# Optimization experiments

Measured on AMD Instinct MI355X. Metric: run time of the kernel, lower is better.

## Reference

```python
import jax, jax.numpy as jnp
import numpy as np

N = 100000   # nodes
E = 1600000  # edges (avg degree 16)
B = 64       # graphs in batch
D_IN = 64
D = 64       # d_model


def setup_inputs() -> dict:
    key = jax.random.key(0)
    ks = jax.random.split(key, 12)
    inp = {}
    inp["x_raw"] = jax.random.normal(ks[0], (N, D_IN), dtype=jnp.float32)
    inp["edge_index"] = jax.random.randint(ks[1], (2, E), 0, N)
    inp["batch"] = jnp.sort(jax.random.randint(ks[2], (N,), 0, B))
    # SAGEConv params per layer: lin_l (weight+bias, applied to neighbor mean),
    # lin_r (weight only, applied to root) -- PyG defaults.
    dins = [D_IN, D, D]
    for i, din in enumerate(dins):
        scale = 1.0 / np.sqrt(din)
        inp[f"Wl{i}"] = jax.random.normal(ks[3 + 3 * i], (D, din), dtype=jnp.float32) * scale
        inp[f"bl{i}"] = jnp.zeros((D,), dtype=jnp.float32)
        inp[f"Wr{i}"] = jax.random.normal(ks[4 + 3 * i], (D, din), dtype=jnp.float32) * scale
    return inp


def _sage_conv(x, src, dst, Wl, bl, Wr):
    """PyG SAGEConv(normalize=True): mean-aggregate neighbors, lin_l + lin_r, L2 norm."""
    msg = jax.ops.segment_sum(x[src], dst, num_segments=N)          # [N, d_in]
    deg = jax.ops.segment_sum(jnp.ones((src.shape[0],), x.dtype), dst, num_segments=N)
    mean = msg / jnp.maximum(deg, 1.0)[:, None]
    out = mean @ Wl.T + bl + x @ Wr.T                               # [N, D]
    nrm = jnp.sqrt(jnp.sum(out * out, axis=-1, keepdims=True))
    return out / jnp.maximum(nrm, 1e-12)


def reference(x_raw, edge_index, batch, Wl0, bl0, Wr0, Wl1, bl1, Wr1, Wl2, bl2, Wr2):
    src, dst = edge_index[0], edge_index[1]
    # dropout is identity in eval mode
    h = jax.nn.relu(_sage_conv(x_raw, src, dst, Wl0, bl0, Wr0))
    h = jax.nn.relu(_sage_conv(h, src, dst, Wl1, bl1, Wr1))
    h = jax.nn.relu(_sage_conv(h, src, dst, Wl2, bl2, Wr2))
    # readout='sum': scatter-sum over batch ids -> [B, D]
    return jax.ops.segment_sum(h, batch, num_segments=B)
```

## Files before the change

### kernel.cpp

```cpp
#include <hip/hip_runtime.h>

#define DFEAT 64

typedef __attribute__((ext_vector_type(8))) short bf16x8;
typedef __attribute__((ext_vector_type(4))) float f32x4;

__device__ __forceinline__ float bfhi(unsigned int u) {
    return __builtin_bit_cast(float, u & 0xFFFF0000u);
}
__device__ __forceinline__ float bflo(unsigned int u) {
    return __builtin_bit_cast(float, u << 16);
}
__device__ __forceinline__ unsigned short f2bf(float f) {
    unsigned int u = __builtin_bit_cast(unsigned int, f);
    u += 0x7FFFu + ((u >> 16) & 1u);
    return (unsigned short)(u >> 16);
}

__global__ void __launch_bounds__(256)
cvt_bf16_kernel(const float* __restrict__ in, unsigned short* __restrict__ outb,
                int n4) {
    int i = blockIdx.x * 256 + threadIdx.x;
    if (i >= n4) return;
    const float4 v = reinterpret_cast<const float4*>(in)[i];
    uint2 p;
    p.x = (unsigned int)f2bf(v.x) | ((unsigned int)f2bf(v.y) << 16);
    p.y = (unsigned int)f2bf(v.z) | ((unsigned int)f2bf(v.w) << 16);
    reinterpret_cast<uint2*>(outb)[i] = p;
}

__global__ void __launch_bounds__(256)
wfrag_cvt_kernel(const float* __restrict__ Wl, const float* __restrict__ Wr,
                 unsigned short* __restrict__ wfrag) {
    const int i4 = blockIdx.x * 256 + threadIdx.x;
    if (i4 >= 1024) return;
    const float4 wl = reinterpret_cast<const float4*>(Wl)[i4];
    const float4 wr = reinterpret_cast<const float4*>(Wr)[i4];
    const int feat = i4 >> 4;
    const int n = feat >> 4, cc = feat & 15;
    const int k0 = (i4 & 15) << 2;
    const int qq = (k0 >> 3) & 3, tl = k0 >> 5, j0 = k0 & 7;
    const int lofs = (qq * 16 + cc) * 8 + j0;
    uint2 pl, pr;
    pl.x = (unsigned int)f2bf(wl.x) | ((unsigned int)f2bf(wl.y) << 16);
    pl.y = (unsigned int)f2bf(wl.z) | ((unsigned int)f2bf(wl.w) << 16);
    pr.x = (unsigned int)f2bf(wr.x) | ((unsigned int)f2bf(wr.y) << 16);
    pr.y = (unsigned int)f2bf(wr.z) | ((unsigned int)f2bf(wr.w) << 16);
    *reinterpret_cast<uint2*>(&wfrag[(n * 4 + tl) * 512 + lofs]) = pl;
    *reinterpret_cast<uint2*>(&wfrag[(n * 4 + 2 + tl) * 512 + lofs]) = pr;
}


__global__ void __launch_bounds__(256)
bucket_hist_kernel(const int* __restrict__ dsts, int* __restrict__ bhist, int E) {
    __shared__ int h[512];
    const int tid = threadIdx.x;
    h[tid] = 0; h[tid + 256] = 0;
    __syncthreads();
    for (int e = blockIdx.x * 256 + tid; e < E; e += gridDim.x * 256)
        atomicAdd(&h[dsts[e] >> 8], 1);
    __syncthreads();
    for (int b = tid; b < 512; b += 256)
        if (h[b]) atomicAdd(&bhist[b], h[b]);
}

__global__ void __launch_bounds__(256)
bucket_scan_kernel(const int* __restrict__ bhist, int* __restrict__ bbase,
                   int* __restrict__ bcur) {
    __shared__ int sm[512];
    const int tid = threadIdx.x;
    sm[tid] = bhist[tid]; sm[tid + 256] = bhist[tid + 256];
    __syncthreads();
    for (int s = 1; s < 512; s <<= 1) {
        int a0 = (tid >= s) ? sm[tid - s] : 0;
        int a1 = sm[tid + 256 - s];
        __syncthreads();
        sm[tid] += a0; sm[tid + 256] += a1;
        __syncthreads();
    }
    for (int b = tid; b < 512; b += 256) {
        int excl = b ? sm[b - 1] : 0;
        bbase[b] = excl; bcur[b] = excl;
    }
    if (tid == 0) bbase[512] = sm[511];
}

#define BIN_CH 2048
__global__ void __launch_bounds__(256)
bin_kernel(const int* __restrict__ srcs, const int* __restrict__ dsts,
           int* __restrict__ bcur, unsigned int* __restrict__ pairbuf, int E) {
    __shared__ int hist[512];
    __shared__ int sscan[512];
    __shared__ int gbase[512];
    __shared__ unsigned int staged[BIN_CH];
    __shared__ unsigned short sbkt[BIN_CH];

    const int tid = threadIdx.x;
    const int base = blockIdx.x * BIN_CH;
    const int chcnt = min(BIN_CH, E - base);

    hist[tid] = 0; hist[tid + 256] = 0;
    __syncthreads();

    unsigned int pk[8];
    unsigned short bb[8], rr[8];
#pragma unroll
    for (int k = 0; k < 8; ++k) {
        int i = k * 256 + tid;
        if (i < chcnt) {
            int e = base + i;
            int d = dsts[e];
            int s = srcs[e];
            int b = d >> 8;
            int r = atomicAdd(&hist[b], 1);
            pk[k] = ((unsigned int)(d & 255) << 24) | (unsigned int)s;
            bb[k] = (unsigned short)b;
            rr[k] = (unsigned short)r;
        } else {
            bb[k] = 0xFFFFu;
        }
    }
    __syncthreads();

    sscan[tid] = hist[tid]; sscan[tid + 256] = hist[tid + 256];
    __syncthreads();
    for (int s = 1; s < 512; s <<= 1) {
        int a0 = (tid >= s) ? sscan[tid - s] : 0;
        int a1 = sscan[tid + 256 - s];
        __syncthreads();
        sscan[tid] += a0; sscan[tid + 256] += a1;
        __syncthreads();
    }

    for (int b = tid; b < 512; b += 256) {
        int c = hist[b];
        gbase[b] = c ? atomicAdd(&bcur[b], c) : 0;
    }
    __syncthreads();

#pragma unroll
    for (int k = 0; k < 8; ++k) {
        if (bb[k] != 0xFFFFu) {
            int b = bb[k];
            int lpos = (b ? sscan[b - 1] : 0) + rr[k];
            staged[lpos] = pk[k];
            sbkt[lpos] = (unsigned short)b;
        }
    }
    __syncthreads();

    for (int i = tid; i < chcnt; i += 256) {
        int b = sbkt[i];
        int excl = b ? sscan[b - 1] : 0;
        pairbuf[gbase[b] + (i - excl)] = staged[i];
    }
}

__global__ void __launch_bounds__(256)
bucket_fill_kernel(const unsigned int* __restrict__ pairbuf,
                   const int* __restrict__ bbase,
                   int* __restrict__ rowptr, int* __restrict__ col,
                   int N, int E) {
    __shared__ int hist[256];
    __shared__ int scan_[256];
    __shared__ int cur[256];

    const int tid = threadIdx.x;
    const int b = blockIdx.x;
    const int node0 = b << 8;
    const int bb0 = bbase[b];
    const int cnt = bbase[b + 1] - bb0;

    hist[tid] = 0;
    __syncthreads();
    for (int i = tid; i < cnt; i += 256)
        atomicAdd(&hist[pairbuf[bb0 + i] >> 24], 1);
    __syncthreads();

    scan_[tid] = hist[tid];
    __syncthreads();
    for (int s = 1; s < 256; s <<= 1) {
        int a = (tid >= s) ? scan_[tid - s] : 0;
        __syncthreads();
        scan_[tid] += a;
        __syncthreads();
    }
    int excl = tid ? scan_[tid - 1] : 0;
    if (node0 + tid < N) rowptr[node0 + tid] = bb0 + excl;
    if (b == 0 && tid == 0) rowptr[N] = E;
    cur[tid] = bb0 + excl;
    __syncthreads();

    for (int i = tid; i < cnt; i += 256) {
        unsigned int p = pairbuf[bb0 + i];
        int pos = atomicAdd(&cur[p >> 24], 1);
        col[pos] = (int)(p & 0xFFFFFFu);
    }
}

__global__ void __launch_bounds__(256, 8)
fused_sage_kernel(const unsigned short* __restrict__ xb,
                  const int* __restrict__ rowptr, const int* __restrict__ col,
                  const unsigned short* __restrict__ wfrag,
                  const float* __restrict__ bl,
                  unsigned short* __restrict__ h_out,
                  const int* __restrict__ batch, float* __restrict__ out,
                  int n_nodes, int final_layer) {
    __shared__ f32x4 part[1024];

    const int tid = threadIdx.x;
    const int w = tid >> 6;
    const int lane = tid & 63;
    const int c = lane & 15;
    const int q = lane >> 4;

    const int base = blockIdx.x << 4;
    const bool valid = (base + c) < n_nodes;
    const int node = valid ? (base + c) : (n_nodes - 1);

    const uint4* rows4 = reinterpret_cast<const uint4*>(xb);
    const int st = rowptr[node];
    const int deg = valid ? (rowptr[node + 1] - st) : 0;

    float accA[8], accB[8];
#pragma unroll
    for (int j = 0; j < 8; ++j) { accA[j] = 0.f; accB[j] = 0.f; }

    if (deg > w) {
        const int dm1 = deg - 1;
        const int* cp = col + st;
        int c0 = cp[w];
        uint4 a0 = rows4[(size_t)c0 * 8 + q];
        uint4 b0 = rows4[(size_t)c0 * 8 + 4 + q];
        int c1 = cp[min(w + 4, dm1)];
        for (int j = w; j < deg; j += 4) {
            const int c2 = cp[min(j + 8, dm1)];
            const uint4 a1 = rows4[(size_t)c1 * 8 + q];
            const uint4 b1 = rows4[(size_t)c1 * 8 + 4 + q];
            accA[0] += bflo(a0.x); accA[1] += bfhi(a0.x);
            accA[2] += bflo(a0.y); accA[3] += bfhi(a0.y);
            accA[4] += bflo(a0.z); accA[5] += bfhi(a0.z);
            accA[6] += bflo(a0.w); accA[7] += bfhi(a0.w);
            accB[0] += bflo(b0.x); accB[1] += bfhi(b0.x);
            accB[2] += bflo(b0.y); accB[3] += bfhi(b0.y);
            accB[4] += bflo(b0.z); accB[5] += bfhi(b0.z);
            accB[6] += bflo(b0.w); accB[7] += bfhi(b0.w);
            a0 = a1; b0 = b1; c1 = c2;
        }
    }
    part[(w * 4 + 0) * 64 + lane] = (f32x4){accA[0], accA[1], accA[2], accA[3]};
    part[(w * 4 + 1) * 64 + lane] = (f32x4){accA[4], accA[5], accA[6], accA[7]};
    part[(w * 4 + 2) * 64 + lane] = (f32x4){accB[0], accB[1], accB[2], accB[3]};
    part[(w * 4 + 3) * 64 + lane] = (f32x4){accB[4], accB[5], accB[6], accB[7]};
    __syncthreads();

    if (w != 0) return;

    f32x4 sA0 = part[0 * 64 + lane]; f32x4 sA1 = part[1 * 64 + lane];
    f32x4 sB0 = part[2 * 64 + lane]; f32x4 sB1 = part[3 * 64 + lane];
#pragma unroll
    for (int ww = 1; ww < 4; ++ww) {
        sA0 += part[(ww * 4 + 0) * 64 + lane];
        sA1 += part[(ww * 4 + 1) * 64 + lane];
        sB0 += part[(ww * 4 + 2) * 64 + lane];
        sB1 += part[(ww * 4 + 3) * 64 + lane];
    }

    const float inv = (deg > 0) ? (1.0f / (float)deg) : 0.0f;
    bf16x8 F0, F1;
#pragma unroll
    for (int j = 0; j < 4; ++j) {
        F0[j]     = (short)f2bf(sA0[j] * inv);
        F0[4 + j] = (short)f2bf(sA1[j] * inv);
        F1[j]     = (short)f2bf(sB0[j] * inv);
        F1[4 + j] = (short)f2bf(sB1[j] * inv);
    }
    const uint4* xrow = reinterpret_cast<const uint4*>(&xb[(size_t)node * 64]);
    const bf16x8 F2 = __builtin_bit_cast(bf16x8, xrow[q]);
    const bf16x8 F3 = __builtin_bit_cast(bf16x8, xrow[4 + q]);

    const bf16x8* fragp = reinterpret_cast<const bf16x8*>(wfrag);
    f32x4 acc[4];
#pragma unroll
    for (int n = 0; n < 4; ++n) acc[n] = (f32x4){0.f, 0.f, 0.f, 0.f};

#pragma unroll
    for (int n = 0; n < 4; ++n) {
        bf16x8 w0 = fragp[(n * 4 + 0) * 64 + lane];
        bf16x8 w1 = fragp[(n * 4 + 1) * 64 + lane];
        bf16x8 w2 = fragp[(n * 4 + 2) * 64 + lane];
        bf16x8 w3 = fragp[(n * 4 + 3) * 64 + lane];
        acc[n] = __builtin_amdgcn_mfma_f32_16x16x32_bf16(w0, F0, acc[n], 0, 0, 0);
        acc[n] = __builtin_amdgcn_mfma_f32_16x16x32_bf16(w1, F1, acc[n], 0, 0, 0);
        acc[n] = __builtin_amdgcn_mfma_f32_16x16x32_bf16(w2, F2, acc[n], 0, 0, 0);
        acc[n] = __builtin_amdgcn_mfma_f32_16x16x32_bf16(w3, F3, acc[n], 0, 0, 0);
    }

    float v[4][4];
    float ss = 0.f;
#pragma unroll
    for (int n = 0; n < 4; ++n) {
        const float4 b4 = reinterpret_cast<const float4*>(bl)[n * 4 + q];
        v[n][0] = acc[n][0] + b4.x;
        v[n][1] = acc[n][1] + b4.y;
        v[n][2] = acc[n][2] + b4.z;
        v[n][3] = acc[n][3] + b4.w;
#pragma unroll
        for (int r = 0; r < 4; ++r) ss += v[n][r] * v[n][r];
    }
    ss += __shfl_xor(ss, 16, 64);
    ss += __shfl_xor(ss, 32, 64);
    const float nrm = 1.0f / fmaxf(sqrtf(ss), 1e-12f);

    if (!final_layer) {
        if (valid) {
            uint2* dst = reinterpret_cast<uint2*>(&h_out[(size_t)(base + c) * 64]);
#pragma unroll
            for (int n = 0; n < 4; ++n) {
                float o0 = fmaxf(v[n][0] * nrm, 0.f), o1 = fmaxf(v[n][1] * nrm, 0.f);
                float o2 = fmaxf(v[n][2] * nrm, 0.f), o3 = fmaxf(v[n][3] * nrm, 0.f);
                uint2 p;
                p.x = (unsigned int)f2bf(o0) | ((unsigned int)f2bf(o1) << 16);
                p.y = (unsigned int)f2bf(o2) | ((unsigned int)f2bf(o3) << 16);
                dst[n * 4 + q] = p;
            }
        }
    } else {
        float o[4][4];
#pragma unroll
        for (int n = 0; n < 4; ++n)
#pragma unroll
            for (int r = 0; r < 4; ++r)
                o[n][r] = valid ? fmaxf(v[n][r] * nrm, 0.f) : 0.f;

        const int lastn = min(base + 15, n_nodes - 1);
        const int gb0 = batch[base];
        if (gb0 == batch[lastn]) {
#pragma unroll
            for (int n = 0; n < 4; ++n)
#pragma unroll
                for (int r = 0; r < 4; ++r) {
                    float s = o[n][r];
                    s += __shfl_xor(s, 1, 64);
                    s += __shfl_xor(s, 2, 64);
                    s += __shfl_xor(s, 4, 64);
                    s += __shfl_xor(s, 8, 64);
                    if (c == 0)
                        atomicAdd(&out[(size_t)gb0 * DFEAT + n * 16 + q * 4 + r], s);
                }
        } else {
            if (valid) {
                const int gb = batch[base + c];
#pragma unroll
                for (int n = 0; n < 4; ++n)
#pragma unroll
                    for (int r = 0; r < 4; ++r)
                        atomicAdd(&out[(size_t)gb * DFEAT + n * 16 + q * 4 + r], o[n][r]);
            }
        }
    }
}

extern "C" void kernel_launch(void* const* d_in, const int* in_sizes, int n_in,
                              void* d_out, int out_size, void* d_ws, size_t ws_size,
                              hipStream_t stream) {
    const float* x_raw = (const float*)d_in[0];
    const int*   eidx  = (const int*)d_in[1];
    const int*   batch = (const int*)d_in[2];
    const float* Wl0 = (const float*)d_in[3];
    const float* bl0 = (const float*)d_in[4];
    const float* Wr0 = (const float*)d_in[5];
    const float* Wl1 = (const float*)d_in[6];
    const float* bl1 = (const float*)d_in[7];
    const float* Wr1 = (const float*)d_in[8];
    const float* Wl2 = (const float*)d_in[9];
    const float* bl2 = (const float*)d_in[10];
    const float* Wr2 = (const float*)d_in[11];

    const int N = in_sizes[0] / DFEAT;
    const int E = in_sizes[1] / 2;
    const int* srcs = eidx;
    const int* dsts = eidx + E;
    float* out = (float*)d_out;

    const int NB = (N + 255) >> 8;

    char* ws = (char*)d_ws;
    auto align512 = [](size_t v) { return (v + 511) & ~(size_t)511; };
    size_t off = 0;
    int* rowptr = (int*)(ws + off); off += align512(((size_t)N + 1) * 4);
    int* col    = (int*)(ws + off); off += align512((size_t)E * 4);
    int* bhist  = (int*)(ws + off); off += align512(512 * 4);
    int* bbase  = (int*)(ws + off); off += align512(513 * 4);
    int* bcur   = (int*)(ws + off); off += align512(512 * 4);
    unsigned short* wfrag0 = (unsigned short*)(ws + off); off += align512(8192 * 2);
    unsigned short* wfrag1 = (unsigned short*)(ws + off); off += align512(8192 * 2);
    unsigned short* wfrag2 = (unsigned short*)(ws + off); off += align512(8192 * 2);
    unsigned short* xb = (unsigned short*)(ws + off); off += align512((size_t)N * DFEAT * 2);
    unsigned short* hA = (unsigned short*)(ws + off); off += align512((size_t)N * DFEAT * 2);
    unsigned short* hB = (unsigned short*)(ws + off);
    unsigned int* pairbuf = (unsigned int*)hA;

    hipMemsetAsync(bhist, 0, 512 * 4, stream);
    hipMemsetAsync(out, 0, (size_t)out_size * 4, stream);

    const int n4 = N * DFEAT / 4;
    cvt_bf16_kernel<<<(n4 + 255) / 256, 256, 0, stream>>>(x_raw, xb, n4);
    wfrag_cvt_kernel<<<4, 256, 0, stream>>>(Wl0, Wr0, wfrag0);
    wfrag_cvt_kernel<<<4, 256, 0, stream>>>(Wl1, Wr1, wfrag1);
    wfrag_cvt_kernel<<<4, 256, 0, stream>>>(Wl2, Wr2, wfrag2);

    bucket_hist_kernel<<<512, 256, 0, stream>>>(dsts, bhist, E);
    bucket_scan_kernel<<<1, 256, 0, stream>>>(bhist, bbase, bcur);
    bin_kernel<<<(E + BIN_CH - 1) / BIN_CH, 256, 0, stream>>>(srcs, dsts, bcur, pairbuf, E);
    bucket_fill_kernel<<<NB, 256, 0, stream>>>(pairbuf, bbase, rowptr, col, N, E);

    const int tiles = (N + 15) / 16;

    fused_sage_kernel<<<tiles, 256, 0, stream>>>(xb, rowptr, col, wfrag0, bl0,
                                                 hA, nullptr, nullptr, N, 0);
    fused_sage_kernel<<<tiles, 256, 0, stream>>>(hA, rowptr, col, wfrag1, bl1,
                                                 hB, nullptr, nullptr, N, 0);
    fused_sage_kernel<<<tiles, 256, 0, stream>>>(hB, rowptr, col, wfrag2, bl2,
                                                 nullptr, batch, out, N, 1);
}
```

Before: 360.7 us.

## Assign one wavefront per node for neighbor gather with shuffled indices

The aggregation is restructured so that each of 16 wavefronts in a 1024-thread block owns one destination node. Its 64 lanes load the node's neighbor indices at once and broadcast them with shuffles, gathering 4 neighbors per step with 8-byte loads. Means are reduced by cross-lane xor shuffles and written bf16 into a small swizzled LDS tile, which wave 0 reads directly as MFMA fragments. This replaces the old scheme of 4 waves splitting every node's neighbor list, along with its large LDS partial-sum reduction, to increase memory-level parallelism and shrink LDS. The risk is that only 1 of 16 waves runs the MFMA and epilogue, and 1024-thread blocks with a low-degree unrolled path may leave lanes idle.

```diff
diff --git a/kernel.cpp b/kernel.cpp
--- a/kernel.cpp
+++ b/kernel.cpp
@@ -15,6 +15,12 @@
     unsigned int u = __builtin_bit_cast(unsigned int, f);
     u += 0x7FFFu + ((u >> 16) & 1u);
     return (unsigned short)(u >> 16);
+}
+__device__ __forceinline__ float4 upk4(uint2 v) {
+    float4 r;
+    r.x = bflo(v.x); r.y = bfhi(v.x);
+    r.z = bflo(v.y); r.w = bfhi(v.y);
+    return r;
 }
 
 __global__ void __launch_bounds__(256)
@@ -198,7 +204,7 @@
     }
 }
 
-__global__ void __launch_bounds__(256, 8)
+__global__ void __launch_bounds__(1024, 2)
 fused_sage_kernel(const unsigned short* __restrict__ xb,
                   const int* __restrict__ rowptr, const int* __restrict__ col,
                   const unsigned short* __restrict__ wfrag,
@@ -206,75 +212,97 @@
                   unsigned short* __restrict__ h_out,
                   const int* __restrict__ batch, float* __restrict__ out,
                   int n_nodes, int final_layer) {
-    __shared__ f32x4 part[1024];
+    __shared__ uint2 meanL[256];
 
     const int tid = threadIdx.x;
-    const int w = tid >> 6;
+    const int ww = tid >> 6;
     const int lane = tid & 63;
+    const int r = lane >> 4;
     const int c = lane & 15;
-    const int q = lane >> 4;
 
     const int base = blockIdx.x << 4;
+    const int node16 = base + ww;
+    const uint2* x2 = reinterpret_cast<const uint2*>(xb);
+
+    int st = 0, deg = 0;
+    if (node16 < n_nodes) { st = rowptr[node16]; deg = rowptr[node16 + 1] - st; }
+
+    const int swz = (c ^ ((ww & 7) << 1));
+
+    if (deg == 0) {
+        if (r == 0) meanL[ww * 16 + swz] = make_uint2(0, 0);
+    } else {
+        int nb = col[st + min(lane, deg - 1)];
+        float4 acc = make_float4(0, 0, 0, 0);
+
+#pragma unroll
+        for (int k = 0; k < 4; ++k) {
+            int i = 4 * k + r;
+            int qn = __shfl(nb, min(i, deg - 1), 64);
+            float4 v = upk4(x2[(size_t)qn * 16 + c]);
+            float m = (i < deg) ? 1.0f : 0.0f;
+            acc.x += v.x * m; acc.y += v.y * m; acc.z += v.z * m; acc.w += v.w * m;
+        }
+        if (deg > 16) {
+#pragma unroll
+            for (int k = 4; k < 8; ++k) {
+                int i = 4 * k + r;
+                int qn = __shfl(nb, min(i, deg - 1), 64);
+                float4 v = upk4(x2[(size_t)qn * 16 + c]);
+                float m = (i < deg) ? 1.0f : 0.0f;
+                acc.x += v.x * m; acc.y += v.y * m; acc.z += v.z * m; acc.w += v.w * m;
+            }
+        }
+        if (deg > 32) {
+#pragma unroll
+            for (int k = 8; k < 16; ++k) {
+                int i = 4 * k + r;
+                int qn = __shfl(nb, min(i, deg - 1), 64);
+                float4 v = upk4(x2[(size_t)qn * 16 + c]);
+                float m = (i < deg) ? 1.0f : 0.0f;
+                acc.x += v.x * m; acc.y += v.y * m; acc.z += v.z * m; acc.w += v.w * m;
+            }
+        }
+        for (int b64 = 64; b64 < deg; b64 += 64) {
+            int cnt = deg - b64;
+            int nb2 = col[st + b64 + min(lane, cnt - 1)];
+#pragma unroll
+            for (int k = 0; k < 16; ++k) {
+                int i = 4 * k + r;
+                int qn = __shfl(nb2, min(i, cnt - 1), 64);
+                float4 v = upk4(x2[(size_t)qn * 16 + c]);
+                float m = (i < cnt) ? 1.0f : 0.0f;
+                acc.x += v.x * m; acc.y += v.y * m; acc.z += v.z * m; acc.w += v.w * m;
+            }
+        }
+
+#pragma unroll
+        for (int off = 16; off <= 32; off <<= 1) {
+            acc.x += __shfl_xor(acc.x, off, 64);
+            acc.y += __shfl_xor(acc.y, off, 64);
+            acc.z += __shfl_xor(acc.z, off, 64);
+            acc.w += __shfl_xor(acc.w, off, 64);
+        }
+        const float inv = 1.0f / (float)deg;
+        if (r == 0) {
+            uint2 p;
+            p.x = (unsigned int)f2bf(acc.x * inv) | ((unsigned int)f2bf(acc.y * inv) << 16);
+            p.y = (unsigned int)f2bf(acc.z * inv) | ((unsigned int)f2bf(acc.w * inv) << 16);
+            meanL[ww * 16 + swz] = p;
+        }
+    }
+    __syncthreads();
+
+    if (ww != 0) return;
+
+    const int q = r;
     const bool valid = (base + c) < n_nodes;
     const int node = valid ? (base + c) : (n_nodes - 1);
 
-    const uint4* rows4 = reinterpret_cast<const uint4*>(xb);
-    const int st = rowptr[node];
-    const int deg = valid ? (rowptr[node + 1] - st) : 0;
-
-    float accA[8], accB[8];
-#pragma unroll
-    for (int j = 0; j < 8; ++j) { accA[j] = 0.f; accB[j] = 0.f; }
-
-    if (deg > w) {
-        const int dm1 = deg - 1;
-        const int* cp = col + st;
-        int c0 = cp[w];
-        uint4 a0 = rows4[(size_t)c0 * 8 + q];
-        uint4 b0 = rows4[(size_t)c0 * 8 + 4 + q];
-        int c1 = cp[min(w + 4, dm1)];
-        for (int j = w; j < deg; j += 4) {
-            const int c2 = cp[min(j + 8, dm1)];
-            const uint4 a1 = rows4[(size_t)c1 * 8 + q];
-            const uint4 b1 = rows4[(size_t)c1 * 8 + 4 + q];
-            accA[0] += bflo(a0.x); accA[1] += bfhi(a0.x);
-            accA[2] += bflo(a0.y); accA[3] += bfhi(a0.y);
-            accA[4] += bflo(a0.z); accA[5] += bfhi(a0.z);
-            accA[6] += bflo(a0.w); accA[7] += bfhi(a0.w);
-            accB[0] += bflo(b0.x); accB[1] += bfhi(b0.x);
-            accB[2] += bflo(b0.y); accB[3] += bfhi(b0.y);
-            accB[4] += bflo(b0.z); accB[5] += bfhi(b0.z);
-            accB[6] += bflo(b0.w); accB[7] += bfhi(b0.w);
-            a0 = a1; b0 = b1; c1 = c2;
-        }
-    }
-    part[(w * 4 + 0) * 64 + lane] = (f32x4){accA[0], accA[1], accA[2], accA[3]};
-    part[(w * 4 + 1) * 64 + lane] = (f32x4){accA[4], accA[5], accA[6], accA[7]};
-    part[(w * 4 + 2) * 64 + lane] = (f32x4){accB[0], accB[1], accB[2], accB[3]};
-    part[(w * 4 + 3) * 64 + lane] = (f32x4){accB[4], accB[5], accB[6], accB[7]};
-    __syncthreads();
-
-    if (w != 0) return;
-
-    f32x4 sA0 = part[0 * 64 + lane]; f32x4 sA1 = part[1 * 64 + lane];
-    f32x4 sB0 = part[2 * 64 + lane]; f32x4 sB1 = part[3 * 64 + lane];
-#pragma unroll
-    for (int ww = 1; ww < 4; ++ww) {
-        sA0 += part[(ww * 4 + 0) * 64 + lane];
-        sA1 += part[(ww * 4 + 1) * 64 + lane];
-        sB0 += part[(ww * 4 + 2) * 64 + lane];
-        sB1 += part[(ww * 4 + 3) * 64 + lane];
-    }
-
-    const float inv = (deg > 0) ? (1.0f / (float)deg) : 0.0f;
-    bf16x8 F0, F1;
-#pragma unroll
-    for (int j = 0; j < 4; ++j) {
-        F0[j]     = (short)f2bf(sA0[j] * inv);
-        F0[4 + j] = (short)f2bf(sA1[j] * inv);
-        F1[j]     = (short)f2bf(sB0[j] * inv);
-        F1[4 + j] = (short)f2bf(sB1[j] * inv);
-    }
+    const uint4* mean4 = reinterpret_cast<const uint4*>(meanL);
+    const int x8 = c & 7;
+    const bf16x8 F0 = __builtin_bit_cast(bf16x8, mean4[c * 8 + (q ^ x8)]);
+    const bf16x8 F1 = __builtin_bit_cast(bf16x8, mean4[c * 8 + ((4 + q) ^ x8)]);
     const uint4* xrow = reinterpret_cast<const uint4*>(&xb[(size_t)node * 64]);
     const bf16x8 F2 = __builtin_bit_cast(bf16x8, xrow[q]);
     const bf16x8 F3 = __builtin_bit_cast(bf16x8, xrow[4 + q]);
@@ -296,17 +324,13 @@
         acc[n] = __builtin_amdgcn_mfma_f32_16x16x32_bf16(w3, F3, acc[n], 0, 0, 0);
     }
 
-    float v[4][4];
     float ss = 0.f;
 #pragma unroll
     for (int n = 0; n < 4; ++n) {
         const float4 b4 = reinterpret_cast<const float4*>(bl)[n * 4 + q];
-        v[n][0] = acc[n][0] + b4.x;
-        v[n][1] = acc[n][1] + b4.y;
-        v[n][2] = acc[n][2] + b4.z;
-        v[n][3] = acc[n][3] + b4.w;
-#pragma unroll
-        for (int r = 0; r < 4; ++r) ss += v[n][r] * v[n][r];
+        acc[n][0] += b4.x; acc[n][1] += b4.y; acc[n][2] += b4.z; acc[n][3] += b4.w;
+#pragma unroll
+        for (int rr = 0; rr < 4; ++rr) ss += acc[n][rr] * acc[n][rr];
     }
     ss += __shfl_xor(ss, 16, 64);
     ss += __shfl_xor(ss, 32, 64);
@@ -317,8 +341,8 @@
             uint2* dst = reinterpret_cast<uint2*>(&h_out[(size_t)(base + c) * 64]);
 #pragma unroll
             for (int n = 0; n < 4; ++n) {
-                float o0 = fmaxf(v[n][0] * nrm, 0.f), o1 = fmaxf(v[n][1] * nrm, 0.f);
-                float o2 = fmaxf(v[n][2] * nrm, 0.f), o3 = fmaxf(v[n][3] * nrm, 0.f);
+                float o0 = fmaxf(acc[n][0] * nrm, 0.f), o1 = fmaxf(acc[n][1] * nrm, 0.f);
+                float o2 = fmaxf(acc[n][2] * nrm, 0.f), o3 = fmaxf(acc[n][3] * nrm, 0.f);
                 uint2 p;
                 p.x = (unsigned int)f2bf(o0) | ((unsigned int)f2bf(o1) << 16);
                 p.y = (unsigned int)f2bf(o2) | ((unsigned int)f2bf(o3) << 16);
@@ -326,27 +350,20 @@
             }
         }
     } else {
-        float o[4][4];
-#pragma unroll
-        for (int n = 0; n < 4; ++n)
-#pragma unroll
-            for (int r = 0; r < 4; ++r)
-                o[n][r] = valid ? fmaxf(v[n][r] * nrm, 0.f) : 0.f;
-
         const int lastn = min(base + 15, n_nodes - 1);
         const int gb0 = batch[base];
         if (gb0 == batch[lastn]) {
 #pragma unroll
             for (int n = 0; n < 4; ++n)
 #pragma unroll
-                for (int r = 0; r < 4; ++r) {
-                    float s = o[n][r];
+                for (int rr = 0; rr < 4; ++rr) {
+                    float s = valid ? fmaxf(acc[n][rr] * nrm, 0.f) : 0.f;
                     s += __shfl_xor(s, 1, 64);
                     s += __shfl_xor(s, 2, 64);
                     s += __shfl_xor(s, 4, 64);
                     s += __shfl_xor(s, 8, 64);
                     if (c == 0)
-                        atomicAdd(&out[(size_t)gb0 * DFEAT + n * 16 + q * 4 + r], s);
+                        atomicAdd(&out[(size_t)gb0 * DFEAT + n * 16 + q * 4 + rr], s);
                 }
         } else {
             if (valid) {
@@ -354,8 +371,9 @@
 #pragma unroll
                 for (int n = 0; n < 4; ++n)
 #pragma unroll
-                    for (int r = 0; r < 4; ++r)
-                        atomicAdd(&out[(size_t)gb * DFEAT + n * 16 + q * 4 + r], o[n][r]);
+                    for (int rr = 0; rr < 4; ++rr)
+                        atomicAdd(&out[(size_t)gb * DFEAT + n * 16 + q * 4 + rr],
+                                  fmaxf(acc[n][rr] * nrm, 0.f));
             }
         }
     }
@@ -417,10 +435,10 @@
 
     const int tiles = (N + 15) / 16;
 
-    fused_sage_kernel<<<tiles, 256, 0, stream>>>(xb, rowptr, col, wfrag0, bl0,
-                                                 hA, nullptr, nullptr, N, 0);
-    fused_sage_kernel<<<tiles, 256, 0, stream>>>(hA, rowptr, col, wfrag1, bl1,
-                                                 hB, nullptr, nullptr, N, 0);
-    fused_sage_kernel<<<tiles, 256, 0, stream>>>(hB, rowptr, col, wfrag2, bl2,
-                                                 nullptr, batch, out, N, 1);
-}
+    fused_sage_kernel<<<tiles, 1024, 0, stream>>>(xb, rowptr, col, wfrag0, bl0,
+                                                  hA, nullptr, nullptr, N, 0);
+    fused_sage_kernel<<<tiles, 1024, 0, stream>>>(hA, rowptr, col, wfrag1, bl1,
+                                                  hB, nullptr, nullptr, N, 0);
+    fused_sage_kernel<<<tiles, 1024, 0, stream>>>(hB, rowptr, col, wfrag2, bl2,
+                                                  nullptr, batch, out, N, 1);
+}
```

Result: slower. 403.3 us (+11.8%).

## Assign one 16-node tile per wavefront instead of splitting edges across four waves

Applied to the files above, without the earlier changes.

Each wavefront now handles its own 16-node tile and walks every neighbor of its nodes. This replaces the old scheme, where four waves split a tile's edges and reduced their partial sums through shared memory. The shared-memory partial buffer, the block barrier and the idle waves in the MFMA epilogue are all removed, so every wave now does transform work. In exchange each wave runs a longer serial gather loop with only a two-deep prefetch. Per-wave latency hiding for the irregular row loads then depends more on having many waves resident.

```diff
diff --git a/kernel.cpp b/kernel.cpp
--- a/kernel.cpp
+++ b/kernel.cpp
@@ -206,15 +206,16 @@
                   unsigned short* __restrict__ h_out,
                   const int* __restrict__ batch, float* __restrict__ out,
                   int n_nodes, int final_layer) {
-    __shared__ f32x4 part[1024];
-
     const int tid = threadIdx.x;
-    const int w = tid >> 6;
+    const int tiles = (n_nodes + 15) >> 4;
+    const int tile = blockIdx.x * 4 + (tid >> 6);
+    if (tile >= tiles) return;
+
     const int lane = tid & 63;
     const int c = lane & 15;
     const int q = lane >> 4;
 
-    const int base = blockIdx.x << 4;
+    const int base = tile << 4;
     const bool valid = (base + c) < n_nodes;
     const int node = valid ? (base + c) : (n_nodes - 1);
 
@@ -226,15 +227,15 @@
 #pragma unroll
     for (int j = 0; j < 8; ++j) { accA[j] = 0.f; accB[j] = 0.f; }
 
-    if (deg > w) {
+    if (deg > 0) {
         const int dm1 = deg - 1;
         const int* cp = col + st;
-        int c0 = cp[w];
+        int c0 = cp[0];
         uint4 a0 = rows4[(size_t)c0 * 8 + q];
         uint4 b0 = rows4[(size_t)c0 * 8 + 4 + q];
-        int c1 = cp[min(w + 4, dm1)];
-        for (int j = w; j < deg; j += 4) {
-            const int c2 = cp[min(j + 8, dm1)];
+        int c1 = cp[min(1, dm1)];
+        for (int j = 0; j < deg; ++j) {
+            const int c2 = cp[min(j + 2, dm1)];
             const uint4 a1 = rows4[(size_t)c1 * 8 + q];
             const uint4 b1 = rows4[(size_t)c1 * 8 + 4 + q];
             accA[0] += bflo(a0.x); accA[1] += bfhi(a0.x);
@@ -248,32 +249,13 @@
             a0 = a1; b0 = b1; c1 = c2;
         }
     }
-    part[(w * 4 + 0) * 64 + lane] = (f32x4){accA[0], accA[1], accA[2], accA[3]};
-    part[(w * 4 + 1) * 64 + lane] = (f32x4){accA[4], accA[5], accA[6], accA[7]};
-    part[(w * 4 + 2) * 64 + lane] = (f32x4){accB[0], accB[1], accB[2], accB[3]};
-    part[(w * 4 + 3) * 64 + lane] = (f32x4){accB[4], accB[5], accB[6], accB[7]};
-    __syncthreads();
-
-    if (w != 0) return;
-
-    f32x4 sA0 = part[0 * 64 + lane]; f32x4 sA1 = part[1 * 64 + lane];
-    f32x4 sB0 = part[2 * 64 + lane]; f32x4 sB1 = part[3 * 64 + lane];
-#pragma unroll
-    for (int ww = 1; ww < 4; ++ww) {
-        sA0 += part[(ww * 4 + 0) * 64 + lane];
-        sA1 += part[(ww * 4 + 1) * 64 + lane];
-        sB0 += part[(ww * 4 + 2) * 64 + lane];
-        sB1 += part[(ww * 4 + 3) * 64 + lane];
-    }
 
     const float inv = (deg > 0) ? (1.0f / (float)deg) : 0.0f;
     bf16x8 F0, F1;
 #pragma unroll
-    for (int j = 0; j < 4; ++j) {
-        F0[j]     = (short)f2bf(sA0[j] * inv);
-        F0[4 + j] = (short)f2bf(sA1[j] * inv);
-        F1[j]     = (short)f2bf(sB0[j] * inv);
-        F1[4 + j] = (short)f2bf(sB1[j] * inv);
+    for (int j = 0; j < 8; ++j) {
+        F0[j] = (short)f2bf(accA[j] * inv);
+        F1[j] = (short)f2bf(accB[j] * inv);
     }
     const uint4* xrow = reinterpret_cast<const uint4*>(&xb[(size_t)node * 64]);
     const bf16x8 F2 = __builtin_bit_cast(bf16x8, xrow[q]);
@@ -415,12 +397,13 @@
     bin_kernel<<<(E + BIN_CH - 1) / BIN_CH, 256, 0, stream>>>(srcs, dsts, bcur, pairbuf, E);
     bucket_fill_kernel<<<NB, 256, 0, stream>>>(pairbuf, bbase, rowptr, col, N, E);
 
-    const int tiles = (N + 15) / 16;
-
-    fused_sage_kernel<<<tiles, 256, 0, stream>>>(xb, rowptr, col, wfrag0, bl0,
-                                                 hA, nullptr, nullptr, N, 0);
-    fused_sage_kernel<<<tiles, 256, 0, stream>>>(hA, rowptr, col, wfrag1, bl1,
-                                                 hB, nullptr, nullptr, N, 0);
-    fused_sage_kernel<<<tiles, 256, 0, stream>>>(hB, rowptr, col, wfrag2, bl2,
-                                                 nullptr, batch, out, N, 1);
-}
+    const int tiles    = (N + 15) / 16;
+    const int xfBlocks = (tiles + 3) / 4;
+
+    fused_sage_kernel<<<xfBlocks, 256, 0, stream>>>(xb, rowptr, col, wfrag0, bl0,
+                                                    hA, nullptr, nullptr, N, 0);
+    fused_sage_kernel<<<xfBlocks, 256, 0, stream>>>(hA, rowptr, col, wfrag1, bl1,
+                                                    hB, nullptr, nullptr, N, 0);
+    fused_sage_kernel<<<xfBlocks, 256, 0, stream>>>(hB, rowptr, col, wfrag2, bl2,
+                                                    nullptr, batch, out, N, 1);
+}
```

After: 322.6 us. 10.6% less time.
